# Performance work log

Hardware: AMD Instinct MI355X
Metric: run time of the kernel (lower is better)

Reference implementation:

```python
import jax, jax.numpy as jnp
import numpy as np

VERY_LARGE_NUMBER = 1e10
NEG_SLOPE = 0.01  # torch leaky_relu default


def setup_inputs() -> dict:
    key = jax.random.key(0)
    k1, k2, k3, k4 = jax.random.split(key, 4)
    N, D, DEG, K, H = 100000, 64, 16, 32, 128
    E = N * DEG
    node_feature = jax.random.normal(k1, (N, D), dtype=jnp.float32)
    # MLP params: Linear(2D -> H), leaky_relu, Linear(H -> 1)
    W1 = jax.random.normal(k2, (2 * D, H), dtype=jnp.float32) * 0.05
    b1 = jnp.zeros((H,), dtype=jnp.float32)
    W2 = jax.random.normal(k3, (H, 1), dtype=jnp.float32) * 0.05
    b2 = jnp.zeros((1,), dtype=jnp.float32)
    # attack edges: each ally node receives DEG messages (uniform degree,
    # sorted by dst -> matches DGL degree-bucketed mailbox ordering)
    dst = jnp.repeat(jnp.arange(N, dtype=jnp.int32), DEG)
    src = jax.random.randint(k4, (E,), 0, N, dtype=jnp.int32)
    return {"node_feature": node_feature, "W1": W1, "b1": b1, "W2": W2,
            "b2": b2, "src": src, "dst": dst, "maximum_num_enemy": K}


def reference(node_feature, W1, b1, W2, b2, src, dst, maximum_num_enemy):
    N = node_feature.shape[0]
    E = dst.shape[0]
    # message: gather dst (ally) and src (enemy) features, concat, MLP -> scalar per edge
    x = jnp.concatenate([node_feature[dst], node_feature[src]], axis=-1)  # [E, 2D]
    h = jax.nn.leaky_relu(x @ W1 + b1, negative_slope=NEG_SLOPE)          # [E, H]
    attack_argument_edge = (h @ W2 + b2)[:, 0]                            # [E]
    # reduce: scatter into padded mailbox [N, maximum_num_enemy];
    # slot = rank of edge within its (sorted) dst segment
    slot = jnp.arange(E, dtype=jnp.int32) - jnp.searchsorted(dst, dst, side='left').astype(jnp.int32)
    out = jnp.full((N, maximum_num_enemy), -VERY_LARGE_NUMBER, dtype=jnp.float32)
    out = out.at[dst, slot].set(attack_argument_edge)
    return out
```

## Files before the change

kernel.cpp:

```cpp
#include <hip/hip_runtime.h>
#include <hip/hip_bf16.h>

typedef __attribute__((ext_vector_type(8))) __bf16 bf16x8;
typedef __attribute__((ext_vector_type(4))) float f32x4;

#if __has_builtin(__builtin_amdgcn_sad_u8)
__device__ __forceinline__ unsigned sad8(unsigned a, unsigned b, unsigned acc) {
    return __builtin_amdgcn_sad_u8(a, b, acc);
}
#else
__device__ __forceinline__ unsigned sad8(unsigned a, unsigned b, unsigned acc) {
    #pragma unroll
    for (int i = 0; i < 4; ++i) {
        int xa = (a >> (8 * i)) & 255, xb = (b >> (8 * i)) & 255;
        acc += (unsigned)((xa > xb) ? (xa - xb) : (xb - xa));
    }
    return acc;
}
#endif

__global__ void prep_w1_kernel(const float* __restrict__ W1,
                               __bf16* __restrict__ W1t) {
    int i = blockIdx.x * 256 + threadIdx.x;
    int c = i >> 7;
    int k = i & 127;
    W1t[i] = (__bf16)W1[k * 128 + c];
}

__global__ void prep_kernel(const float* __restrict__ W1,
                            const float* __restrict__ b1,
                            const float* __restrict__ W2,
                            __bf16* __restrict__ W1pt,
                            float* __restrict__ b1p,
                            float* __restrict__ w2p,
                            int* __restrict__ npout,
                            float* __restrict__ qs) {
    __shared__ int perm_inv_s[128];
    __shared__ int wcnt[2];
    __shared__ float wmax[2];
    const int tid  = threadIdx.x;
    const int lane = tid & 63;
    const int w    = tid >> 6;
    bool pos = false;
    int rank = 0;
    if (tid < 128) {
        const float w2 = W2[tid];
        pos = (w2 > 0.f);
        unsigned long long bal = __ballot(pos);
        rank = __popcll(bal & ((1ull << lane) - 1ull));
        int cnt = __popcll(bal);
        float m = __builtin_fabsf(w2);
        #pragma unroll
        for (int d = 1; d < 64; d <<= 1) m = fmaxf(m, __shfl_xor(m, d, 64));
        if (lane == 0) { wcnt[w] = cnt; wmax[w] = m; }
    }
    __syncthreads();
    if (tid < 128) {
        const int npv   = wcnt[0] + wcnt[1];
        const int basep = (w == 1) ? wcnt[0] : 0;
        const int negb  = (w == 1) ? (64 - wcnt[0]) : 0;
        const int p = pos ? (basep + rank) : (npv + negb + (lane - rank));
        perm_inv_s[p] = tid;
    }
    __syncthreads();

    const int i = blockIdx.x * 256 + tid;
    const int j = i >> 7;
    const int k = i & 127;
    const int c = perm_inv_s[(j & 15) * 8 + (j >> 4)];
    W1pt[i] = (__bf16)W1[k * 128 + c];
    if (k == 0) { b1p[j] = b1[c]; w2p[j] = W2[c]; }
    if (i == 0) {
        float mm = fmaxf(wmax[0], wmax[1]);
        float s  = (mm > 0.f) ? (6.0f * mm / 120.0f) : 1.0f;
        qs[0] = 1.0f / s;
        qs[1] = 0.495f * s;
        *npout = wcnt[0] + wcnt[1];
    }
}

__global__ void precomp_kernel(const float* __restrict__ nf,
                               const float* __restrict__ b1p,
                               const float* __restrict__ w2p,
                               const float* __restrict__ b2,
                               const __bf16* __restrict__ W1pt,
                               const float* __restrict__ qs,
                               unsigned char* __restrict__ A1u,
                               unsigned char* __restrict__ A2q,
                               float* __restrict__ R1,
                               float* __restrict__ R2,
                               float* __restrict__ out,
                               int T2, int K) {
    const int lane = threadIdx.x & 63;
    const int wid  = threadIdx.x >> 6;
    const int mode = wid & 1;
    const int cc   = lane & 15;
    const int kg   = lane >> 4;
    const int koff = mode ? 64 : 0;
    const float inv_s = qs[0];

    bf16x8 bfrag[8][2];
    #pragma unroll
    for (int ct = 0; ct < 8; ++ct) {
        const __bf16* colp = W1pt + (ct * 16 + cc) * 128 + koff + kg * 8;
        bfrag[ct][0] = *(const bf16x8*)(colp);
        bfrag[ct][1] = *(const bf16x8*)(colp + 32);
    }
    float bwv[8], wv[8], qm[8];
    #pragma unroll
    for (int ct = 0; ct < 8; ++ct) {
        const int col = ct * 16 + cc;
        const float w2v = w2p[col];
        wv[ct]  = w2v;
        bwv[ct] = mode ? 0.f : b1p[col];
        const float m8 = inv_s * __builtin_fabsf(w2v);
        qm[ct] = mode ? (-m8 * (1.0f / 85.0f)) : m8;
    }
    const float radd = mode ? 0.f : b2[0];
    const int oddadd = (cc & 1) ? 4 : 0;

    const int stride = gridDim.x * 2;
    for (int g = blockIdx.x * 2 + (wid >> 1); g < T2; g += stride) {
        const float* ap = nf + ((long)g * 16 + cc) * 64 + kg * 8;
        f32x4 lo0 = *(const f32x4*)(ap);
        f32x4 hi0 = *(const f32x4*)(ap + 4);
        f32x4 lo1 = *(const f32x4*)(ap + 32);
        f32x4 hi1 = *(const f32x4*)(ap + 36);
        bf16x8 a0, a1;
        #pragma unroll
        for (int j = 0; j < 4; ++j) {
            a0[j] = (__bf16)lo0[j]; a0[4 + j] = (__bf16)hi0[j];
            a1[j] = (__bf16)lo1[j]; a1[4 + j] = (__bf16)hi1[j];
        }

        f32x4 acc[8];
        #pragma unroll
        for (int ct = 0; ct < 8; ++ct) acc[ct] = (f32x4){0.f, 0.f, 0.f, 0.f};
        #pragma unroll
        for (int ct = 0; ct < 8; ++ct) {
            acc[ct] = __builtin_amdgcn_mfma_f32_16x16x32_bf16(a0, bfrag[ct][0], acc[ct], 0, 0, 0);
            acc[ct] = __builtin_amdgcn_mfma_f32_16x16x32_bf16(a1, bfrag[ct][1], acc[ct], 0, 0, 0);
        }

        #pragma unroll
        for (int r = 0; r < 4; ++r) {
            const long n = (long)g * 16 + kg * 4 + r;
            float rs = 0.f;
            if (mode == 0) {
                unsigned ub[8];
                #pragma unroll
                for (int ct = 0; ct < 8; ++ct) {
                    const float raw = acc[ct][r] + bwv[ct];
                    rs = fmaf(raw, wv[ct], rs);
                    float x = fmaf(raw, qm[ct], 128.f);
                    x = fminf(fmaxf(x, 1.f), 254.f);
                    ub[ct] = (unsigned)(x + 0.5f);
                }
                rs += __shfl_xor(rs, 1, 64);
                rs += __shfl_xor(rs, 2, 64);
                rs += __shfl_xor(rs, 4, 64);
                rs += __shfl_xor(rs, 8, 64);
                int2 o;
                o.x = (int)(ub[0] | (ub[1] << 8) | (ub[2] << 16) | (ub[3] << 24));
                o.y = (int)(ub[4] | (ub[5] << 8) | (ub[6] << 16) | (ub[7] << 24));
                *(int2*)(A1u + n * 128 + cc * 8) = o;
                if (cc == 0) R1[n] = 0.505f * rs + radd;
            } else {
                unsigned pk = 0;
                #pragma unroll
                for (int ct = 0; ct < 8; ++ct) {
                    const float raw = acc[ct][r];
                    rs = fmaf(raw, wv[ct], rs);
                    float t = fmaf(raw, qm[ct], 2.00588f);
                    t = fminf(fmaxf(t, 0.f), 3.0f);
                    pk |= ((unsigned)t) << (8 * (ct & 3) + 2 * (ct >> 2) + oddadd);
                }
                rs += __shfl_xor(rs, 1, 64);
                rs += __shfl_xor(rs, 2, 64);
                rs += __shfl_xor(rs, 4, 64);
                rs += __shfl_xor(rs, 8, 64);
                const unsigned ph = (unsigned)__shfl_xor((int)pk, 1, 64);
                const unsigned dwv = pk | ph;
                if (!(cc & 1))
                    *(unsigned*)(A2q + n * 32 + (cc >> 1) * 4) = dwv;
                if (cc == 0) R2[n] = 0.505f * rs;
            }
        }

        if (mode == 0) {
            const f32x4 fill = (f32x4){-1e10f, -1e10f, -1e10f, -1e10f};
            const long node = (long)g * 16 + (lane >> 2);
            float* orow = out + node * K + (lane & 3) * 4;
            *(f32x4*)(orow)      = fill;
            *(f32x4*)(orow + 16) = fill;
        }
    }
}

__global__ void edge_kernel(const unsigned char* __restrict__ A1u,
                            const unsigned char* __restrict__ A2q,
                            const float* __restrict__ R1,
                            const float* __restrict__ R2,
                            const float* __restrict__ qs,
                            const int* __restrict__ npp,
                            const int* __restrict__ src,
                            const int* __restrict__ dst,
                            float* __restrict__ out,
                            int E, int K) {
    const int lane = threadIdx.x & 63;
    const int gw   = blockIdx.x * 4 + (threadIdx.x >> 6);
    const float k0 = qs[1];
    const int np   = *npp;

    unsigned M[32];
    #pragma unroll
    for (int m = 0; m < 32; ++m) {
        const int t = np - 4 * m;
        M[m] = (t >= 4) ? 0xFFFFFFFFu
             : ((t <= 0) ? 0u : (0xFFFFFFFFu >> (8 * (4 - t))));
    }

    const int e = gw * 64 + lane;
    const bool act = (e < E);
    const int dvl = act ? dst[e] : 0;
    const bool okc = !act || (dvl == (e >> 4));
    const bool fast = (__ballot(okc) == ~0ull);
    if (!act) return;

    int dv, slot;
    if (fast) { dv = e >> 4; slot = e & 15; }
    else {
        dv = dvl;
        int lo = 0, hi = e;
        while (lo < hi) {
            int mid = (lo + hi) >> 1;
            if (dst[mid] < dv) lo = mid + 1; else hi = mid;
        }
        slot = e - lo;
    }
    const int se = src[e];

    const unsigned char* bp = A2q + (long)se * 32;
    int4 q0 = *(const int4*)(bp);
    int4 q1 = *(const int4*)(bp + 16);
    const unsigned char* ap_ = A1u + (long)dv * 128;
    unsigned A[32];
    #pragma unroll
    for (int i = 0; i < 8; ++i) {
        int4 t = *(const int4*)(ap_ + i * 16);
        A[4 * i]     = (unsigned)t.x;
        A[4 * i + 1] = (unsigned)t.y;
        A[4 * i + 2] = (unsigned)t.z;
        A[4 * i + 3] = (unsigned)t.w;
    }
    const float r12 = R1[dv] + R2[se];

    unsigned B[8] = {(unsigned)q0.x, (unsigned)q0.y, (unsigned)q0.z, (unsigned)q0.w,
                     (unsigned)q1.x, (unsigned)q1.y, (unsigned)q1.z, (unsigned)q1.w};
    unsigned sall = 0, spl = 0;
    #pragma unroll
    for (int d = 0; d < 8; ++d) {
        const unsigned v = B[d];
        #pragma unroll
        for (int k = 0; k < 4; ++k) {
            unsigned x = (v >> (2 * k)) & 0x03030303u;
            unsigned y = x + (x << 2);
            y = y + (y << 4);
            const unsigned mm = M[4 * d + k];
            const unsigned aa = A[4 * d + k];
            sall = sad8(aa, y, sall);
            spl  = sad8(aa & mm, y & mm, spl);
        }
    }

    const float score = fmaf(k0, 2.0f * (float)spl - (float)sall, r12);
    if (slot < K) out[(long)dv * K + slot] = score;
}

__global__ void attack_kernel_f(
    const float* __restrict__ nf, const float* __restrict__ b1,
    const float* __restrict__ W2, const float* __restrict__ b2,
    const int* __restrict__ src, const int* __restrict__ dst,
    const __bf16* __restrict__ W1t, float* __restrict__ out,
    int T, int K, int DEG)
{
    const int lane = threadIdx.x & 63;
    const int wid  = threadIdx.x >> 6;
    const int row  = lane & 15;
    const int kg   = lane >> 4;

    bf16x8 bfrag[8][4];
    #pragma unroll
    for (int ct = 0; ct < 8; ++ct) {
        const __bf16* colp = W1t + (ct * 16 + row) * 128 + kg * 8;
        #pragma unroll
        for (int kk = 0; kk < 4; ++kk)
            bfrag[ct][kk] = *(const bf16x8*)(colp + kk * 32);
    }
    float b1c[8], w2c[8];
    #pragma unroll
    for (int ct = 0; ct < 8; ++ct) {
        b1c[ct] = b1[ct * 16 + row];
        w2c[ct] = W2[ct * 16 + row];
    }
    const float b2v = b2[0];

    const int wstride = gridDim.x * 4;
    for (int t = blockIdx.x * 4 + wid; t < T; t += wstride) {
        const long eb = (long)t * DEG;
        const int dv = dst[eb];
        const int sv = src[eb + row];
        bf16x8 afrag[4];
        const float* dp = nf + (long)dv * 64 + kg * 8;
        const float* sp = nf + (long)sv * 64 + kg * 8;
        #pragma unroll
        for (int kk = 0; kk < 2; ++kk) {
            f32x4 lo = *(const f32x4*)(dp + kk * 32);
            f32x4 hi = *(const f32x4*)(dp + kk * 32 + 4);
            bf16x8 a;
            #pragma unroll
            for (int j = 0; j < 4; ++j) { a[j] = (__bf16)lo[j]; a[4 + j] = (__bf16)hi[j]; }
            afrag[kk] = a;
        }
        #pragma unroll
        for (int kk = 0; kk < 2; ++kk) {
            f32x4 lo = *(const f32x4*)(sp + kk * 32);
            f32x4 hi = *(const f32x4*)(sp + kk * 32 + 4);
            bf16x8 a;
            #pragma unroll
            for (int j = 0; j < 4; ++j) { a[j] = (__bf16)lo[j]; a[4 + j] = (__bf16)hi[j]; }
            afrag[2 + kk] = a;
        }
        f32x4 acc[8];
        #pragma unroll
        for (int ct = 0; ct < 8; ++ct) acc[ct] = (f32x4){0.f, 0.f, 0.f, 0.f};
        #pragma unroll
        for (int ct = 0; ct < 8; ++ct) {
            #pragma unroll
            for (int kk = 0; kk < 4; ++kk)
                acc[ct] = __builtin_amdgcn_mfma_f32_16x16x32_bf16(
                    afrag[kk], bfrag[ct][kk], acc[ct], 0, 0, 0);
        }
        float part[4] = {0.f, 0.f, 0.f, 0.f};
        #pragma unroll
        for (int ct = 0; ct < 8; ++ct) {
            #pragma unroll
            for (int r = 0; r < 4; ++r) {
                float h = acc[ct][r] + b1c[ct];
                h = fmaxf(h, 0.01f * h);
                part[r] = fmaf(h, w2c[ct], part[r]);
            }
        }
        #pragma unroll
        for (int m = 1; m < 16; m <<= 1) {
            #pragma unroll
            for (int r = 0; r < 4; ++r)
                part[r] += __shfl_xor(part[r], m, 64);
        }
        float* orow = out + (long)dv * K;
        if (row == 0) {
            f32x4 v;
            #pragma unroll
            for (int r = 0; r < 4; ++r) v[r] = part[r] + b2v;
            *(f32x4*)(orow + kg * 4) = v;
            *(f32x4*)(orow + DEG + kg * 4) = (f32x4){-1e10f, -1e10f, -1e10f, -1e10f};
        }
    }
}

extern "C" void kernel_launch(void* const* d_in, const int* in_sizes, int n_in,
                              void* d_out, int out_size, void* d_ws, size_t ws_size,
                              hipStream_t stream) {
    const float* nf  = (const float*)d_in[0];
    const float* W1  = (const float*)d_in[1];
    const float* b1  = (const float*)d_in[2];
    const float* W2  = (const float*)d_in[3];
    const float* b2  = (const float*)d_in[4];
    const int*   src = (const int*)d_in[5];
    const int*   dst = (const int*)d_in[6];
    float* out = (float*)d_out;

    const int H    = in_sizes[2];
    const int twoD = in_sizes[1] / H;
    const int D    = twoD / 2;
    const int N    = in_sizes[0] / D;
    const int E    = in_sizes[5];
    const int DEG  = E / N;
    const int K    = out_size / N;

    const size_t w1_off   = 0;
    const size_t qs_off   = 32768;
    const size_t np_off   = 32784;
    const size_t b1p_off  = 33312;
    const size_t w2p_off  = 33824;
    const size_t A1_off   = 34560;
    const size_t A1_sz    = (size_t)N * 128;
    const size_t A2_off   = A1_off + A1_sz;
    const size_t A2_sz    = (size_t)N * 32;
    const size_t R1_off   = A2_off + A2_sz;
    const size_t R2_off   = R1_off + (size_t)N * sizeof(float);
    const size_t need     = R2_off + (size_t)N * sizeof(float);

    const bool special = (D == 64 && H == 128 && DEG == 16 && K == 32 &&
                          (N % 16) == 0 && (E % 64) == 0 && ws_size >= need);
    if (special) {
        __bf16*        W1pt = (__bf16*)((char*)d_ws + w1_off);
        float*         qs   = (float*)((char*)d_ws + qs_off);
        int*           npp  = (int*)((char*)d_ws + np_off);
        float*         b1p  = (float*)((char*)d_ws + b1p_off);
        float*         w2p  = (float*)((char*)d_ws + w2p_off);
        unsigned char* A1u  = (unsigned char*)d_ws + A1_off;
        unsigned char* A2q  = (unsigned char*)d_ws + A2_off;
        float*         R1   = (float*)((char*)d_ws + R1_off);
        float*         R2   = (float*)((char*)d_ws + R2_off);

        prep_kernel<<<64, 256, 0, stream>>>(W1, b1, W2, W1pt, b1p, w2p,
                                            npp, qs);
        const int T2 = N / 16;
        precomp_kernel<<<512, 256, 0, stream>>>(nf, b1p, w2p, b2, W1pt, qs,
                                                A1u, A2q, R1, R2, out, T2, K);
        const int eblocks = (E + 255) / 256;
        edge_kernel<<<eblocks, 256, 0, stream>>>(A1u, A2q, R1, R2, qs, npp,
                                                 src, dst, out, E, K);
    } else {
        __bf16* W1t = (__bf16*)((char*)d_ws + w1_off);
        prep_w1_kernel<<<(twoD * H + 255) / 256, 256, 0, stream>>>(W1, W1t);
        attack_kernel_f<<<2048, 256, 0, stream>>>(nf, b1, W2, b2, src, dst,
                                                  W1t, out, N, K, DEG);
    }
}
```

Measured before the change: 74.21 us.

## Fold weight prep into precompute and edge kernels, move padding fill to edge kernel

Removes the separate prep kernel launch. Each precompute block now recomputes the W2 sign permutation and quantization scale in shared memory and gathers its bf16 W1 fragments directly from the fp32 weights, and the edge kernel recomputes the scale and positive count itself. The -1e10 padding writes move from the precompute kernel into the edge kernel, which writes the unused second half of each row next to the scores. Precompute is also reorganized so whole blocks handle one mode (1024 blocks split into halves) instead of alternating modes per wave. This saves a launch and some global traffic, but every block now does redundant strided W1 loads and a reduction.

```diff
diff --git a/kernel.cpp b/kernel.cpp
--- a/kernel.cpp
+++ b/kernel.cpp
@@ -27,20 +27,23 @@
     W1t[i] = (__bf16)W1[k * 128 + c];
 }
 
-__global__ void prep_kernel(const float* __restrict__ W1,
-                            const float* __restrict__ b1,
-                            const float* __restrict__ W2,
-                            __bf16* __restrict__ W1pt,
-                            float* __restrict__ b1p,
-                            float* __restrict__ w2p,
-                            int* __restrict__ npout,
-                            float* __restrict__ qs) {
+__global__ void precomp_kernel(const float* __restrict__ nf,
+                               const float* __restrict__ W1,
+                               const float* __restrict__ b1,
+                               const float* __restrict__ W2,
+                               const float* __restrict__ b2,
+                               unsigned char* __restrict__ A1u,
+                               unsigned char* __restrict__ A2q,
+                               float* __restrict__ R1,
+                               float* __restrict__ R2,
+                               int T2) {
     __shared__ int perm_inv_s[128];
     __shared__ int wcnt[2];
     __shared__ float wmax[2];
+    __shared__ float s_inv;
     const int tid  = threadIdx.x;
     const int lane = tid & 63;
-    const int w    = tid >> 6;
+    const int wv   = tid >> 6;
     bool pos = false;
     int rank = 0;
     if (tid < 128) {
@@ -52,75 +55,57 @@
         float m = __builtin_fabsf(w2);
         #pragma unroll
         for (int d = 1; d < 64; d <<= 1) m = fmaxf(m, __shfl_xor(m, d, 64));
-        if (lane == 0) { wcnt[w] = cnt; wmax[w] = m; }
+        if (lane == 0) { wcnt[wv] = cnt; wmax[wv] = m; }
     }
     __syncthreads();
     if (tid < 128) {
         const int npv   = wcnt[0] + wcnt[1];
-        const int basep = (w == 1) ? wcnt[0] : 0;
-        const int negb  = (w == 1) ? (64 - wcnt[0]) : 0;
+        const int basep = (wv == 1) ? wcnt[0] : 0;
+        const int negb  = (wv == 1) ? (64 - wcnt[0]) : 0;
         const int p = pos ? (basep + rank) : (npv + negb + (lane - rank));
         perm_inv_s[p] = tid;
     }
-    __syncthreads();
-
-    const int i = blockIdx.x * 256 + tid;
-    const int j = i >> 7;
-    const int k = i & 127;
-    const int c = perm_inv_s[(j & 15) * 8 + (j >> 4)];
-    W1pt[i] = (__bf16)W1[k * 128 + c];
-    if (k == 0) { b1p[j] = b1[c]; w2p[j] = W2[c]; }
-    if (i == 0) {
+    if (tid == 0) {
         float mm = fmaxf(wmax[0], wmax[1]);
         float s  = (mm > 0.f) ? (6.0f * mm / 120.0f) : 1.0f;
-        qs[0] = 1.0f / s;
-        qs[1] = 0.495f * s;
-        *npout = wcnt[0] + wcnt[1];
-    }
-}
-
-__global__ void precomp_kernel(const float* __restrict__ nf,
-                               const float* __restrict__ b1p,
-                               const float* __restrict__ w2p,
-                               const float* __restrict__ b2,
-                               const __bf16* __restrict__ W1pt,
-                               const float* __restrict__ qs,
-                               unsigned char* __restrict__ A1u,
-                               unsigned char* __restrict__ A2q,
-                               float* __restrict__ R1,
-                               float* __restrict__ R2,
-                               float* __restrict__ out,
-                               int T2, int K) {
-    const int lane = threadIdx.x & 63;
-    const int wid  = threadIdx.x >> 6;
-    const int mode = wid & 1;
-    const int cc   = lane & 15;
-    const int kg   = lane >> 4;
-    const int koff = mode ? 64 : 0;
-    const float inv_s = qs[0];
+        s_inv = 1.0f / s;
+    }
+    __syncthreads();
+
+    const int wid   = tid >> 6;
+    const int cc    = lane & 15;
+    const int kg    = lane >> 4;
+    const int halfg = gridDim.x >> 1;
+    const int mode  = (blockIdx.x >= halfg) ? 1 : 0;
+    const int b0    = mode ? (blockIdx.x - halfg) : blockIdx.x;
+    const int koff  = mode ? 64 : 0;
+    const float inv_s = s_inv;
 
     bf16x8 bfrag[8][2];
+    float bwv[8], wvv[8], qm[8];
     #pragma unroll
     for (int ct = 0; ct < 8; ++ct) {
-        const __bf16* colp = W1pt + (ct * 16 + cc) * 128 + koff + kg * 8;
-        bfrag[ct][0] = *(const bf16x8*)(colp);
-        bfrag[ct][1] = *(const bf16x8*)(colp + 32);
-    }
-    float bwv[8], wv[8], qm[8];
-    #pragma unroll
-    for (int ct = 0; ct < 8; ++ct) {
-        const int col = ct * 16 + cc;
-        const float w2v = w2p[col];
-        wv[ct]  = w2v;
-        bwv[ct] = mode ? 0.f : b1p[col];
+        const int c = perm_inv_s[cc * 8 + ct];
+        const float* wp = W1 + (koff + kg * 8) * 128 + c;
+        bf16x8 f0, f1;
+        #pragma unroll
+        for (int j = 0; j < 8; ++j) {
+            f0[j] = (__bf16)wp[j * 128];
+            f1[j] = (__bf16)wp[(j + 32) * 128];
+        }
+        bfrag[ct][0] = f0;
+        bfrag[ct][1] = f1;
+        const float w2v = W2[c];
+        wvv[ct] = w2v;
+        bwv[ct] = mode ? 0.f : b1[c];
         const float m8 = inv_s * __builtin_fabsf(w2v);
         qm[ct] = mode ? (-m8 * (1.0f / 85.0f)) : m8;
     }
     const float radd = mode ? 0.f : b2[0];
     const int oddadd = (cc & 1) ? 4 : 0;
 
-    const int stride = gridDim.x * 2;
-    for (int g = blockIdx.x * 2 + (wid >> 1); g < T2; g += stride) {
+    const int stride = halfg * 4;
+    for (int g = b0 * 4 + wid; g < T2; g += stride) {
         const float* ap = nf + ((long)g * 16 + cc) * 64 + kg * 8;
         f32x4 lo0 = *(const f32x4*)(ap);
         f32x4 hi0 = *(const f32x4*)(ap + 4);
@@ -151,7 +136,7 @@
                 #pragma unroll
                 for (int ct = 0; ct < 8; ++ct) {
                     const float raw = acc[ct][r] + bwv[ct];
-                    rs = fmaf(raw, wv[ct], rs);
+                    rs = fmaf(raw, wvv[ct], rs);
                     float x = fmaf(raw, qm[ct], 128.f);
                     x = fminf(fmaxf(x, 1.f), 254.f);
                     ub[ct] = (unsigned)(x + 0.5f);
@@ -170,7 +155,7 @@
                 #pragma unroll
                 for (int ct = 0; ct < 8; ++ct) {
                     const float raw = acc[ct][r];
-                    rs = fmaf(raw, wv[ct], rs);
+                    rs = fmaf(raw, wvv[ct], rs);
                     float t = fmaf(raw, qm[ct], 2.00588f);
                     t = fminf(fmaxf(t, 0.f), 3.0f);
                     pk |= ((unsigned)t) << (8 * (ct & 3) + 2 * (ct >> 2) + oddadd);
@@ -186,14 +171,6 @@
                 if (cc == 0) R2[n] = 0.505f * rs;
             }
         }
-
-        if (mode == 0) {
-            const f32x4 fill = (f32x4){-1e10f, -1e10f, -1e10f, -1e10f};
-            const long node = (long)g * 16 + (lane >> 2);
-            float* orow = out + node * K + (lane & 3) * 4;
-            *(f32x4*)(orow)      = fill;
-            *(f32x4*)(orow + 16) = fill;
-        }
     }
 }
 
@@ -201,16 +178,37 @@
                             const unsigned char* __restrict__ A2q,
                             const float* __restrict__ R1,
                             const float* __restrict__ R2,
-                            const float* __restrict__ qs,
-                            const int* __restrict__ npp,
+                            const float* __restrict__ W2,
                             const int* __restrict__ src,
                             const int* __restrict__ dst,
                             float* __restrict__ out,
                             int E, int K) {
-    const int lane = threadIdx.x & 63;
-    const int gw   = blockIdx.x * 4 + (threadIdx.x >> 6);
-    const float k0 = qs[1];
-    const int np   = *npp;
+    __shared__ int wcnt[2];
+    __shared__ float wmax[2];
+    __shared__ int s_np;
+    __shared__ float s_k0;
+    const int tid  = threadIdx.x;
+    const int lane = tid & 63;
+    if (tid < 128) {
+        const float w2 = W2[tid];
+        const bool pos = (w2 > 0.f);
+        unsigned long long bal = __ballot(pos);
+        int cnt = __popcll(bal);
+        float m = __builtin_fabsf(w2);
+        #pragma unroll
+        for (int d = 1; d < 64; d <<= 1) m = fmaxf(m, __shfl_xor(m, d, 64));
+        if (lane == 0) { wcnt[tid >> 6] = cnt; wmax[tid >> 6] = m; }
+    }
+    __syncthreads();
+    if (tid == 0) {
+        float mm = fmaxf(wmax[0], wmax[1]);
+        float s  = (mm > 0.f) ? (6.0f * mm / 120.0f) : 1.0f;
+        s_np = wcnt[0] + wcnt[1];
+        s_k0 = 0.495f * s;
+    }
+    __syncthreads();
+    const int np   = s_np;
+    const float k0 = s_k0;
 
     unsigned M[32];
     #pragma unroll
@@ -220,7 +218,8 @@
              : ((t <= 0) ? 0u : (0xFFFFFFFFu >> (8 * (4 - t))));
     }
 
-    const int e = gw * 64 + lane;
+    const int gw = blockIdx.x * 4 + (tid >> 6);
+    const int e  = gw * 64 + lane;
     const bool act = (e < E);
     const int dvl = act ? dst[e] : 0;
     const bool okc = !act || (dvl == (e >> 4));
@@ -228,6 +227,7 @@
     if (!act) return;
 
     int dv, slot;
+    bool lastseg = false;
     if (fast) { dv = e >> 4; slot = e & 15; }
     else {
         dv = dvl;
@@ -237,6 +237,7 @@
             if (dst[mid] < dv) lo = mid + 1; else hi = mid;
         }
         slot = e - lo;
+        lastseg = (e + 1 >= E) || (dst[e + 1] != dv);
     }
     const int se = src[e];
 
@@ -274,7 +275,15 @@
     }
 
     const float score = fmaf(k0, 2.0f * (float)spl - (float)sall, r12);
-    if (slot < K) out[(long)dv * K + slot] = score;
+    float* orow = out + (long)dv * K;
+    if (fast) {
+        orow[slot]      = score;
+        orow[16 + slot] = -1e10f;
+    } else {
+        if (slot < K) orow[slot] = score;
+        if (lastseg)
+            for (int q = slot + 1; q < K; ++q) orow[q] = -1e10f;
+    }
 }
 
 __global__ void attack_kernel_f(
@@ -388,42 +397,30 @@
     const int DEG  = E / N;
     const int K    = out_size / N;
 
-    const size_t w1_off   = 0;
-    const size_t qs_off   = 32768;
-    const size_t np_off   = 32784;
-    const size_t b1p_off  = 33312;
-    const size_t w2p_off  = 33824;
-    const size_t A1_off   = 34560;
-    const size_t A1_sz    = (size_t)N * 128;
-    const size_t A2_off   = A1_off + A1_sz;
-    const size_t A2_sz    = (size_t)N * 32;
-    const size_t R1_off   = A2_off + A2_sz;
-    const size_t R2_off   = R1_off + (size_t)N * sizeof(float);
-    const size_t need     = R2_off + (size_t)N * sizeof(float);
+    const size_t A1_off = 0;
+    const size_t A1_sz  = (size_t)N * 128;
+    const size_t A2_off = A1_off + A1_sz;
+    const size_t A2_sz  = (size_t)N * 32;
+    const size_t R1_off = A2_off + A2_sz;
+    const size_t R2_off = R1_off + (size_t)N * sizeof(float);
+    const size_t need   = R2_off + (size_t)N * sizeof(float);
 
     const bool special = (D == 64 && H == 128 && DEG == 16 && K == 32 &&
                           (N % 16) == 0 && (E % 64) == 0 && ws_size >= need);
     if (special) {
-        __bf16*        W1pt = (__bf16*)((char*)d_ws + w1_off);
-        float*         qs   = (float*)((char*)d_ws + qs_off);
-        int*           npp  = (int*)((char*)d_ws + np_off);
-        float*         b1p  = (float*)((char*)d_ws + b1p_off);
-        float*         w2p  = (float*)((char*)d_ws + w2p_off);
-        unsigned char* A1u  = (unsigned char*)d_ws + A1_off;
-        unsigned char* A2q  = (unsigned char*)d_ws + A2_off;
-        float*         R1   = (float*)((char*)d_ws + R1_off);
-        float*         R2   = (float*)((char*)d_ws + R2_off);
-
-        prep_kernel<<<64, 256, 0, stream>>>(W1, b1, W2, W1pt, b1p, w2p,
-                                            npp, qs);
+        unsigned char* A1u = (unsigned char*)d_ws + A1_off;
+        unsigned char* A2q = (unsigned char*)d_ws + A2_off;
+        float*         R1  = (float*)((char*)d_ws + R1_off);
+        float*         R2  = (float*)((char*)d_ws + R2_off);
+
         const int T2 = N / 16;
-        precomp_kernel<<<512, 256, 0, stream>>>(nf, b1p, w2p, b2, W1pt, qs,
-                                                A1u, A2q, R1, R2, out, T2, K);
+        precomp_kernel<<<1024, 256, 0, stream>>>(nf, W1, b1, W2, b2,
+                                                 A1u, A2q, R1, R2, T2);
         const int eblocks = (E + 255) / 256;
-        edge_kernel<<<eblocks, 256, 0, stream>>>(A1u, A2q, R1, R2, qs, npp,
+        edge_kernel<<<eblocks, 256, 0, stream>>>(A1u, A2q, R1, R2, W2,
                                                  src, dst, out, E, K);
     } else {
-        __bf16* W1t = (__bf16*)((char*)d_ws + w1_off);
+        __bf16* W1t = (__bf16*)d_ws;
         prep_w1_kernel<<<(twoD * H + 255) / 256, 256, 0, stream>>>(W1, W1t);
         attack_kernel_f<<<2048, 256, 0, stream>>>(nf, b1, W2, b2, src, dst,
                                                   W1t, out, N, K, DEG);
```

After: 90.52 us. +22.0%, slower.
